# Kernel tuning notes

Hardware: AMD Instinct MI355X
Metric: run time of the kernel (lower is better)

The kernel has to match this reference:

```python
import jax, jax.numpy as jnp
import numpy as np
import math

H = 256; W = 256
NUM_CURVES = 256
NUM_SAMPLES = 32
NUM_BEZIERS = 2
BDEG = 5            # Bernstein degree used by the module (bezier_degree+1)
CTRL_STRIDE = 5     # bezier_degree+1; segments share endpoints, wrap (closed curve)
N_CTRL = NUM_BEZIERS * CTRL_STRIDE   # 10 control points per closed curve
PIX_CHUNK = 512
CHOLESKY_BOUND = jnp.array([0.5, 0.0, 0.5], jnp.float32)


def _bernstein():
    # t in linspace(0.007, 0.993, S) exactly as _update_bernstein_cache
    t = jnp.linspace(0.007, 0.993, NUM_SAMPLES)
    i = jnp.arange(BDEG + 1, dtype=jnp.float32)
    comb = jnp.array([math.comb(BDEG, k) for k in range(BDEG + 1)], jnp.float32)
    return comb * (t[:, None] ** i) * ((1.0 - t[:, None]) ** (BDEG - i))  # [S, BDEG+1]


def _render(control_points, features_dc, cholesky, opacity, depth, background):
    Bmat = _bernstein()
    # closed curve: segment k uses control points (k*5 + j) mod 10, j=0..5
    seg_idx = (jnp.arange(NUM_BEZIERS)[:, None] * CTRL_STRIDE
               + jnp.arange(BDEG + 1)[None, :]) % N_CTRL          # [K, 6]
    seg_ctrl = control_points[:, seg_idx]                          # [N, K, 6, 2]
    pts = jnp.einsum('sj,nkjd->nksd', Bmat, seg_ctrl)              # [N, K, S, 2]
    pts = pts.reshape(NUM_CURVES, -1, 2)                           # [N, Gper, 2]
    gper = pts.shape[1]

    # normalized [-1,1] -> pixel coords
    means = (jnp.tanh(pts) * 0.5 + 0.5) * jnp.array([W, H], jnp.float32)
    means = means.reshape(-1, 2)                                   # [G, 2]

    # 2x2 covariance from lower-triangular Cholesky (per curve)
    c = cholesky + CHOLESKY_BOUND[None, :]                         # l11, l21, l22
    s00 = c[:, 0] ** 2
    s01 = c[:, 0] * c[:, 1]
    s11 = c[:, 1] ** 2 + c[:, 2] ** 2
    det = s00 * s11 - s01 ** 2
    conic = jnp.stack([s11 / det, -s01 / det, s00 / det], -1)      # [N, 3]

    rep = lambda a: jnp.repeat(a, gper, axis=0)
    conic_g = rep(conic)                                           # [G, 3]
    color_g = rep(jax.nn.sigmoid(features_dc))                     # [G, 3]
    alpha_g = rep(jax.nn.sigmoid(opacity))[:, 0]                   # [G]
    depth_g = rep(depth)[:, 0]                                     # [G]

    order = jnp.argsort(depth_g)                                   # front-to-back
    means_s = means[order]
    conic_s = conic_g[order]
    color_s = color_g[order]
    alpha_s = alpha_g[order]

    ys, xs = jnp.meshgrid(jnp.arange(H, dtype=jnp.float32) + 0.5,
                          jnp.arange(W, dtype=jnp.float32) + 0.5, indexing='ij')
    pix = jnp.stack([xs.ravel(), ys.ravel()], -1).reshape(-1, PIX_CHUNK, 2)

    @jax.checkpoint
    def render_chunk(p):                                           # [C,2] -> [C,3]
        dx = p[:, None, 0] - means_s[None, :, 0]
        dy = p[:, None, 1] - means_s[None, :, 1]
        power = (-0.5 * (conic_s[None, :, 0] * dx * dx
                         + conic_s[None, :, 2] * dy * dy)
                 - conic_s[None, :, 1] * dx * dy)
        a = jnp.clip(alpha_s[None, :] * jnp.exp(power), 0.0, 0.999)
        logT = jnp.cumsum(jnp.log1p(-a), axis=1)
        t_excl = jnp.exp(logT - jnp.log1p(-a))   # transmittance before each splat
        rgb = (a * t_excl) @ color_s             # [C, 3]
        return rgb + jnp.exp(logT[:, -1:]) * background[None, :]

    img = jax.lax.map(render_chunk, pix)                           # [P/C, C, 3]
    return jnp.clip(img.reshape(H, W, 3), 0.0, 1.0)


def setup_inputs() -> dict:
    key = jax.random.key(0)
    k1, k2, k3, k4 = jax.random.split(key, 4)
    return {
        "control_points": jax.random.normal(k1, (NUM_CURVES, N_CTRL, 2), jnp.float32),
        "features_dc": jax.random.uniform(k2, (NUM_CURVES, 3), jnp.float32),
        "cholesky": jax.random.uniform(k3, (NUM_CURVES, 3), jnp.float32),
        "opacity": jnp.ones((NUM_CURVES, 1), jnp.float32),
        "depth": jax.random.uniform(k4, (NUM_CURVES, 1), jnp.float32),
        "background": jnp.ones((3,), jnp.float32),
    }


def reference(control_points, features_dc, cholesky, opacity, depth, background):
    return _render(control_points, features_dc, cholesky, opacity, depth, background)
```

## Files before the change

kernel.cpp:

```cpp
#include <hip/hip_runtime.h>
#include <hip/hip_fp16.h>
#include <math.h>

#define NCURVES   256
#define GPER      64
#define NUM_G     (NCURVES*GPER)
#define IMG_W     256
#define IMG_H     256
#define TILE      16
#define TILES_X   (IMG_W/TILE)
#define TILES_Y   (IMG_H/TILE)
#define NTILES    (TILES_X*TILES_Y)
#define REC_F     8

#define A_MIN     3.0e-6f
#define P_CUT     (-12.6f)

#define SEGS      8
#define GSEG      (NUM_G/SEGS)
#define GWAVE     (GSEG/4)

__global__ __launch_bounds__(GPER)
void prep(const float* __restrict__ ctrl,
          const float* __restrict__ features,
          const float* __restrict__ cholesky,
          const float* __restrict__ opacity,
          const float* __restrict__ depth,
          float*       __restrict__ recs,
          unsigned*    __restrict__ bbox)
{
    int c   = blockIdx.x;
    int tid = threadIdx.x;

    float dc = depth[c];
    int r = 0;
    #pragma unroll
    for (int jj = 0; jj < 4; ++jj) {
        int j = tid + jj*64;
        float dj = depth[j];
        r += (dj < dc) || (dj == dc && j < c);
    }
    #pragma unroll
    for (int off = 32; off > 0; off >>= 1) r += __shfl_down(r, off, 64);
    r = __shfl(r, 0, 64);

    float c0 = cholesky[3*c+0] + 0.5f;
    float c1 = cholesky[3*c+1];
    float c2 = cholesky[3*c+2] + 0.5f;
    float s00 = c0*c0;
    float s01 = c0*c1;
    float s11 = c1*c1 + c2*c2;
    float inv = 1.0f / (s00*s11 - s01*s01);
    float A  =  s11*inv;
    float Bc = -s01*inv;
    float Cc =  s00*inv;

    float cr = 1.0f/(1.0f + __expf(-features[3*c+0]));
    float cg = 1.0f/(1.0f + __expf(-features[3*c+1]));
    float cb = 1.0f/(1.0f + __expf(-features[3*c+2]));
    float al = 1.0f/(1.0f + __expf(-opacity[c]));

    float cut = fmaxf(2.0f*(__logf(al) - __logf(A_MIN)), 0.0f);
    float rx = sqrtf(cut * s00);
    float ry = sqrtf(cut * s11);

    int k = tid >> 5;
    int s = tid & 31;
    float t = 0.007f + (float)s * (0.986f/31.0f);
    float u = 1.0f - t;
    float t2=t*t, t3=t2*t, t4=t3*t, t5=t4*t;
    float u2=u*u, u3=u2*u, u4=u3*u, u5=u4*u;
    float w[6] = { u5, 5.0f*t*u4, 10.0f*t2*u3, 10.0f*t3*u2, 5.0f*t4*u, t5 };

    const float* cp = ctrl + c*20;
    float px = 0.0f, py = 0.0f;
    #pragma unroll
    for (int j = 0; j < 6; ++j) {
        int idx = (k*5 + j) % 10;
        px += w[j]*cp[2*idx+0];
        py += w[j]*cp[2*idx+1];
    }
    float mx = (tanhf(px)*0.5f + 0.5f) * (float)IMG_W;
    float my = (tanhf(py)*0.5f + 0.5f) * (float)IMG_H;

    int gi = r*GPER + tid;

    unsigned rg  = (unsigned)__half_as_ushort(__float2half_rn(cr))
                 | ((unsigned)__half_as_ushort(__float2half_rn(cg)) << 16);
    unsigned cbp = (unsigned)__half_as_ushort(__float2half_rn(cb));

    float4* o4 = (float4*)(recs + (size_t)gi*REC_F);
    o4[0] = make_float4(mx, my, A, Bc);
    o4[1] = make_float4(Cc, al, __uint_as_float(rg), __uint_as_float(cbp));

    int tx0 = min(max((int)floorf((mx - rx) * (1.0f/TILE)), 0), TILES_X-1);
    int tx1 = min(max((int)floorf((mx + rx) * (1.0f/TILE)), 0), TILES_X-1);
    int ty0 = min(max((int)floorf((my - ry) * (1.0f/TILE)), 0), TILES_Y-1);
    int ty1 = min(max((int)floorf((my + ry) * (1.0f/TILE)), 0), TILES_Y-1);
    bbox[gi] = (unsigned)tx0 | ((unsigned)ty0<<8) | ((unsigned)tx1<<16) | ((unsigned)ty1<<24);
}

__global__ __launch_bounds__(256)
void render8(const float*    __restrict__ recs,
             const unsigned* __restrict__ bbox,
             float4*         __restrict__ partial)
{
    __shared__ unsigned short flat[GSEG];
    __shared__ unsigned       wn[4];

    int tid   = threadIdx.x;
    int seg   = blockIdx.x & (SEGS-1);
    int tile  = blockIdx.x >> 3;
    int tilex = tile & (TILES_X-1);
    int tiley = tile >> 4;

    int lane = tid & 63;
    int wid  = tid >> 6;
    unsigned long long lmask = (1ull << lane) - 1ull;

    int sbase = seg * GSEG;
    int gwave = wid * GWAVE;

    bool pr[8];
    int cnt = 0;
    {
        unsigned bb[8];
        #pragma unroll
        for (int u = 0; u < 8; ++u)
            bb[u] = bbox[sbase + gwave + u*64 + lane];
        #pragma unroll
        for (int u = 0; u < 8; ++u) {
            unsigned b = bb[u];
            pr[u] = (tilex >= (int)( b        & 0xff)) &
                    (tilex <= (int)((b >> 16) & 0xff)) &
                    (tiley >= (int)((b >>  8) & 0xff)) &
                    (tiley <= (int)((b >> 24) & 0xff));
            cnt += (int)__popcll(__ballot(pr[u] ? 1 : 0));
        }
    }
    if (lane == 0) wn[wid] = (unsigned)cnt;
    __syncthreads();

    unsigned p1 = wn[0], p2 = p1 + wn[1], p3 = p2 + wn[2];
    int total = (int)(p3 + wn[3]);

    if (total) {
        unsigned base = (wid == 0) ? 0u : (wid == 1) ? p1 : (wid == 2) ? p2 : p3;
        int off = 0;
        #pragma unroll
        for (int u = 0; u < 8; ++u) {
            unsigned long long m = __ballot(pr[u] ? 1 : 0);
            if (pr[u])
                flat[base + off + (int)__popcll(m & lmask)] =
                    (unsigned short)(gwave + u*64 + lane);
            off += (int)__popcll(m);
        }
    }
    __syncthreads();

    int ix = tid & (TILE-1);
    int iy = tid >> 4;
    float pxf = (float)(tilex*TILE + ix) + 0.5f;
    float pyf = (float)(tiley*TILE + iy) + 0.5f;

    float T = 1.0f, accr = 0.0f, accg = 0.0f, accb = 0.0f;

    #pragma unroll 2
    for (int j = 0; j < total; ++j) {
        int gl = (int)flat[j];
        const float4* rp = (const float4*)(recs + (size_t)(sbase + gl)*REC_F);
        float4 r0 = rp[0];
        float4 r1 = rp[1];
        float dx = pxf - r0.x;
        float dy = pyf - r0.y;
        float p  = -0.5f*(r0.z*dx*dx + r1.x*dy*dy) - r0.w*dx*dy;
        if (p > P_CUT) {
            float a = fminf(r1.y * __expf(p), 0.999f);
            float wgt = a * T;
            unsigned rg = __float_as_uint(r1.z);
            accr += wgt * __half2float(__ushort_as_half((unsigned short)(rg & 0xffff)));
            accg += wgt * __half2float(__ushort_as_half((unsigned short)(rg >> 16)));
            accb += wgt * __half2float(__ushort_as_half((unsigned short)__float_as_uint(r1.w)));
            T *= (1.0f - a);
        }
    }

    int X = tilex*TILE + ix;
    int Y = tiley*TILE + iy;
    partial[(size_t)seg*(IMG_W*IMG_H) + (size_t)Y*IMG_W + X] =
        make_float4(accr, accg, accb, T);
}

__global__ __launch_bounds__(256)
void combine(const float4* __restrict__ partial,
             const float*  __restrict__ background,
             float*        __restrict__ out)
{
    int p = blockIdx.x * 256 + threadIdx.x;

    float accr = 0.0f, accg = 0.0f, accb = 0.0f, T = 1.0f;
    #pragma unroll
    for (int s = 0; s < SEGS; ++s) {
        float4 q = partial[(size_t)s*(IMG_W*IMG_H) + p];
        accr += T * q.x;
        accg += T * q.y;
        accb += T * q.z;
        T    *= q.w;
    }
    float r = fminf(fmaxf(accr + T*background[0], 0.0f), 1.0f);
    float g = fminf(fmaxf(accg + T*background[1], 0.0f), 1.0f);
    float b = fminf(fmaxf(accb + T*background[2], 0.0f), 1.0f);

    size_t oi = (size_t)p*3;
    out[oi+0] = r;
    out[oi+1] = g;
    out[oi+2] = b;
}

extern "C" void kernel_launch(void* const* d_in, const int* in_sizes, int n_in,
                              void* d_out, int out_size, void* d_ws, size_t ws_size,
                              hipStream_t stream)
{
    const float* ctrl       = (const float*)d_in[0];
    const float* features   = (const float*)d_in[1];
    const float* cholesky   = (const float*)d_in[2];
    const float* opacity    = (const float*)d_in[3];
    const float* depth      = (const float*)d_in[4];
    const float* background = (const float*)d_in[5];
    float* out = (float*)d_out;

    char* w = (char*)d_ws;
    float*    recs    = (float*)   (w);
    unsigned* bboxp   = (unsigned*)(w + 524288);
    float4*   partial = (float4*)  (w + 524288 + 65536);

    prep<<<NCURVES, GPER, 0, stream>>>(ctrl, features, cholesky, opacity, depth,
                                       recs, bboxp);
    render8<<<NTILES*SEGS, 256, 0, stream>>>(recs, bboxp, partial);
    combine<<<(IMG_W*IMG_H)/256, 256, 0, stream>>>(partial, background, out);
}
```

Before: 84.32 us.

## Software-pipeline record loads in render loop and exit early on saturation

The per-tile splat loop now processes records in groups of four, loading the next group into registers while the current group is composited, so global-load latency overlaps with math. The loop stops once every lane in the wave has transmittance below a small epsilon. The render kernel also gets a minimum-occupancy launch bound. The early exit drops contributions below the epsilon and may shift outputs slightly, and the prefetch buffers increase register pressure.

```diff
diff --git a/kernel.cpp b/kernel.cpp
--- a/kernel.cpp
+++ b/kernel.cpp
@@ -15,10 +15,12 @@
 
 #define A_MIN     3.0e-6f
 #define P_CUT     (-12.6f)
+#define T_EPS     1.0e-5f
 
 #define SEGS      8
 #define GSEG      (NUM_G/SEGS)
 #define GWAVE     (GSEG/4)
+#define PF        4
 
 __global__ __launch_bounds__(GPER)
 void prep(const float* __restrict__ ctrl,
@@ -100,7 +102,7 @@
     bbox[gi] = (unsigned)tx0 | ((unsigned)ty0<<8) | ((unsigned)tx1<<16) | ((unsigned)ty1<<24);
 }
 
-__global__ __launch_bounds__(256)
+__global__ __launch_bounds__(256, 4)
 void render8(const float*    __restrict__ recs,
              const unsigned* __restrict__ bbox,
              float4*         __restrict__ partial)
@@ -165,24 +167,51 @@
 
     float T = 1.0f, accr = 0.0f, accg = 0.0f, accb = 0.0f;
 
-    #pragma unroll 2
-    for (int j = 0; j < total; ++j) {
-        int gl = (int)flat[j];
-        const float4* rp = (const float4*)(recs + (size_t)(sbase + gl)*REC_F);
-        float4 r0 = rp[0];
-        float4 r1 = rp[1];
-        float dx = pxf - r0.x;
-        float dy = pyf - r0.y;
-        float p  = -0.5f*(r0.z*dx*dx + r1.x*dy*dy) - r0.w*dx*dy;
-        if (p > P_CUT) {
-            float a = fminf(r1.y * __expf(p), 0.999f);
-            float wgt = a * T;
-            unsigned rg = __float_as_uint(r1.z);
-            accr += wgt * __half2float(__ushort_as_half((unsigned short)(rg & 0xffff)));
-            accg += wgt * __half2float(__ushort_as_half((unsigned short)(rg >> 16)));
-            accb += wgt * __half2float(__ushort_as_half((unsigned short)__float_as_uint(r1.w)));
-            T *= (1.0f - a);
-        }
+    float4 c0[PF], c1[PF], n0[PF], n1[PF];
+
+    #pragma unroll
+    for (int u = 0; u < PF; ++u) {
+        if (u < total) {
+            const float4* rp = (const float4*)
+                (recs + (size_t)(sbase + (int)flat[u])*REC_F);
+            c0[u] = rp[0]; c1[u] = rp[1];
+        }
+    }
+
+    #pragma unroll 1
+    for (int base = 0; base < total; base += PF) {
+        int nb = base + PF;
+        #pragma unroll
+        for (int u = 0; u < PF; ++u) {
+            if (nb + u < total) {
+                const float4* rp = (const float4*)
+                    (recs + (size_t)(sbase + (int)flat[nb + u])*REC_F);
+                n0[u] = rp[0]; n1[u] = rp[1];
+            }
+        }
+        #pragma unroll
+        for (int u = 0; u < PF; ++u) {
+            if (base + u < total) {
+                float4 r0 = c0[u];
+                float4 r1 = c1[u];
+                float dx = pxf - r0.x;
+                float dy = pyf - r0.y;
+                float p  = -0.5f*(r0.z*dx*dx + r1.x*dy*dy) - r0.w*dx*dy;
+                if (p > P_CUT) {
+                    float a = fminf(r1.y * __expf(p), 0.999f);
+                    float wgt = a * T;
+                    unsigned rg = __float_as_uint(r1.z);
+                    accr += wgt * __half2float(__ushort_as_half((unsigned short)(rg & 0xffff)));
+                    accg += wgt * __half2float(__ushort_as_half((unsigned short)(rg >> 16)));
+                    accb += wgt * __half2float(__ushort_as_half((unsigned short)__float_as_uint(r1.w)));
+                    T *= (1.0f - a);
+                }
+            }
+        }
+        #pragma unroll
+        for (int u = 0; u < PF; ++u) { c0[u] = n0[u]; c1[u] = n1[u]; }
+
+        if (!__any(T > T_EPS)) break;
     }
 
     int X = tilex*TILE + ix;
```

Measured after the change: 87.60 us. +3.9%, slower.

## Render 8x8 tiles with per-wave depth quarters and in-block combine

Applied to the files above, without the earlier changes.

Shrinks tiles to 8x8 so each of the four waves in a block covers the same 64 pixels, with each wave taking a quarter of the depth-sorted splats. The four partial results are composited in shared memory, which removes the separate combine kernel and the global partial buffer. Each wave also exits early once every lane's transmittance falls below a small epsilon. In exchange each block scans a quarter of all bboxes per wave, and early termination adds a tiny approximation.

```diff
diff --git a/kernel.cpp b/kernel.cpp
--- a/kernel.cpp
+++ b/kernel.cpp
@@ -7,7 +7,7 @@
 #define NUM_G     (NCURVES*GPER)
 #define IMG_W     256
 #define IMG_H     256
-#define TILE      16
+#define TILE      8
 #define TILES_X   (IMG_W/TILE)
 #define TILES_Y   (IMG_H/TILE)
 #define NTILES    (TILES_X*TILES_Y)
@@ -15,10 +15,10 @@
 
 #define A_MIN     3.0e-6f
 #define P_CUT     (-12.6f)
-
-#define SEGS      8
-#define GSEG      (NUM_G/SEGS)
-#define GWAVE     (GSEG/4)
+#define T_EPS     1.0e-5f
+
+#define WQ        4
+#define GQ        (NUM_G/WQ)
 
 __global__ __launch_bounds__(GPER)
 void prep(const float* __restrict__ ctrl,
@@ -101,74 +101,55 @@
 }
 
 __global__ __launch_bounds__(256)
-void render8(const float*    __restrict__ recs,
-             const unsigned* __restrict__ bbox,
-             float4*         __restrict__ partial)
+void render8x8(const float*    __restrict__ recs,
+               const unsigned* __restrict__ bbox,
+               const float*    __restrict__ background,
+               float*          __restrict__ out)
 {
-    __shared__ unsigned short flat[GSEG];
-    __shared__ unsigned       wn[4];
+    __shared__ unsigned short lst[WQ][GQ];
+    __shared__ float4         pc[WQ][64];
 
     int tid   = threadIdx.x;
-    int seg   = blockIdx.x & (SEGS-1);
-    int tile  = blockIdx.x >> 3;
+    int lane  = tid & 63;
+    int w     = tid >> 6;
+    int tile  = blockIdx.x;
     int tilex = tile & (TILES_X-1);
-    int tiley = tile >> 4;
-
-    int lane = tid & 63;
-    int wid  = tid >> 6;
+    int tiley = tile >> 5;
     unsigned long long lmask = (1ull << lane) - 1ull;
 
-    int sbase = seg * GSEG;
-    int gwave = wid * GWAVE;
-
-    bool pr[8];
+    int gb = w * GQ;
+
     int cnt = 0;
-    {
+    #pragma unroll 1
+    for (int b = 0; b < 8; ++b) {
         unsigned bb[8];
         #pragma unroll
         for (int u = 0; u < 8; ++u)
-            bb[u] = bbox[sbase + gwave + u*64 + lane];
+            bb[u] = bbox[gb + (b*8 + u)*64 + lane];
         #pragma unroll
         for (int u = 0; u < 8; ++u) {
-            unsigned b = bb[u];
-            pr[u] = (tilex >= (int)( b        & 0xff)) &
-                    (tilex <= (int)((b >> 16) & 0xff)) &
-                    (tiley >= (int)((b >>  8) & 0xff)) &
-                    (tiley <= (int)((b >> 24) & 0xff));
-            cnt += (int)__popcll(__ballot(pr[u] ? 1 : 0));
+            unsigned v = bb[u];
+            bool pred = (tilex >= (int)( v        & 0xff)) &
+                        (tilex <= (int)((v >> 16) & 0xff)) &
+                        (tiley >= (int)((v >>  8) & 0xff)) &
+                        (tiley <= (int)((v >> 24) & 0xff));
+            unsigned long long m = __ballot(pred ? 1 : 0);
+            if (pred)
+                lst[w][cnt + (int)__popcll(m & lmask)] =
+                    (unsigned short)((b*8 + u)*64 + lane);
+            cnt += (int)__popcll(m);
         }
     }
-    if (lane == 0) wn[wid] = (unsigned)cnt;
-    __syncthreads();
-
-    unsigned p1 = wn[0], p2 = p1 + wn[1], p3 = p2 + wn[2];
-    int total = (int)(p3 + wn[3]);
-
-    if (total) {
-        unsigned base = (wid == 0) ? 0u : (wid == 1) ? p1 : (wid == 2) ? p2 : p3;
-        int off = 0;
-        #pragma unroll
-        for (int u = 0; u < 8; ++u) {
-            unsigned long long m = __ballot(pr[u] ? 1 : 0);
-            if (pr[u])
-                flat[base + off + (int)__popcll(m & lmask)] =
-                    (unsigned short)(gwave + u*64 + lane);
-            off += (int)__popcll(m);
-        }
-    }
-    __syncthreads();
-
-    int ix = tid & (TILE-1);
-    int iy = tid >> 4;
-    float pxf = (float)(tilex*TILE + ix) + 0.5f;
-    float pyf = (float)(tiley*TILE + iy) + 0.5f;
+
+    float pxf = (float)(tilex*TILE + (lane & 7)) + 0.5f;
+    float pyf = (float)(tiley*TILE + (lane >> 3)) + 0.5f;
 
     float T = 1.0f, accr = 0.0f, accg = 0.0f, accb = 0.0f;
 
     #pragma unroll 2
-    for (int j = 0; j < total; ++j) {
-        int gl = (int)flat[j];
-        const float4* rp = (const float4*)(recs + (size_t)(sbase + gl)*REC_F);
+    for (int j = 0; j < cnt; ++j) {
+        int g = gb + (int)lst[w][j];
+        const float4* rp = (const float4*)(recs + (size_t)g*REC_F);
         float4 r0 = rp[0];
         float4 r1 = rp[1];
         float dx = pxf - r0.x;
@@ -183,38 +164,33 @@
             accb += wgt * __half2float(__ushort_as_half((unsigned short)__float_as_uint(r1.w)));
             T *= (1.0f - a);
         }
-    }
-
-    int X = tilex*TILE + ix;
-    int Y = tiley*TILE + iy;
-    partial[(size_t)seg*(IMG_W*IMG_H) + (size_t)Y*IMG_W + X] =
-        make_float4(accr, accg, accb, T);
-}
-
-__global__ __launch_bounds__(256)
-void combine(const float4* __restrict__ partial,
-             const float*  __restrict__ background,
-             float*        __restrict__ out)
-{
-    int p = blockIdx.x * 256 + threadIdx.x;
-
-    float accr = 0.0f, accg = 0.0f, accb = 0.0f, T = 1.0f;
-    #pragma unroll
-    for (int s = 0; s < SEGS; ++s) {
-        float4 q = partial[(size_t)s*(IMG_W*IMG_H) + p];
-        accr += T * q.x;
-        accg += T * q.y;
-        accb += T * q.z;
-        T    *= q.w;
-    }
-    float r = fminf(fmaxf(accr + T*background[0], 0.0f), 1.0f);
-    float g = fminf(fmaxf(accg + T*background[1], 0.0f), 1.0f);
-    float b = fminf(fmaxf(accb + T*background[2], 0.0f), 1.0f);
-
-    size_t oi = (size_t)p*3;
-    out[oi+0] = r;
-    out[oi+1] = g;
-    out[oi+2] = b;
+        if (!__any(T > T_EPS)) break;
+    }
+
+    pc[w][lane] = make_float4(accr, accg, accb, T);
+    __syncthreads();
+
+    if (w == 0) {
+        float4 a0 = pc[0][lane];
+        float4 a1 = pc[1][lane];
+        float4 a2 = pc[2][lane];
+        float4 a3 = pc[3][lane];
+        float r = a0.x + a0.w*(a1.x + a1.w*(a2.x + a2.w*a3.x));
+        float g = a0.y + a0.w*(a1.y + a1.w*(a2.y + a2.w*a3.y));
+        float b = a0.z + a0.w*(a1.z + a1.w*(a2.z + a2.w*a3.z));
+        float Tt = a0.w * a1.w * a2.w * a3.w;
+
+        r = fminf(fmaxf(r + Tt*background[0], 0.0f), 1.0f);
+        g = fminf(fmaxf(g + Tt*background[1], 0.0f), 1.0f);
+        b = fminf(fmaxf(b + Tt*background[2], 0.0f), 1.0f);
+
+        int X = tilex*TILE + (lane & 7);
+        int Y = tiley*TILE + (lane >> 3);
+        size_t oi = ((size_t)Y*IMG_W + X)*3;
+        out[oi+0] = r;
+        out[oi+1] = g;
+        out[oi+2] = b;
+    }
 }
 
 extern "C" void kernel_launch(void* const* d_in, const int* in_sizes, int n_in,
@@ -230,12 +206,10 @@
     float* out = (float*)d_out;
 
     char* w = (char*)d_ws;
-    float*    recs    = (float*)   (w);
-    unsigned* bboxp   = (unsigned*)(w + 524288);
-    float4*   partial = (float4*)  (w + 524288 + 65536);
+    float*    recs  = (float*)   (w);
+    unsigned* bboxp = (unsigned*)(w + 524288);
 
     prep<<<NCURVES, GPER, 0, stream>>>(ctrl, features, cholesky, opacity, depth,
                                        recs, bboxp);
-    render8<<<NTILES*SEGS, 256, 0, stream>>>(recs, bboxp, partial);
-    combine<<<(IMG_W*IMG_H)/256, 256, 0, stream>>>(partial, background, out);
+    render8x8<<<NTILES, 256, 0, stream>>>(recs, bboxp, background, out);
 }
```

New measurement: 95.28 us. 13.0% more time.

## Stage splat records in shared memory and terminate early on saturated transmittance

Applied to the files above, without the earlier changes.

The render loop now loads blocks of up to 512 candidate splat records cooperatively into LDS, and all pixels read them from there. Before, every thread fetched each record from global memory on its own. It also adds block-level and wave-level early exit once transmittance drops below 1e-5, which skips splats that would contribute almost nothing. The cost is 16KB of extra LDS per block, which may lower occupancy, plus extra barriers. The early exit changes results slightly, since it ignores contributions below the epsilon.

```diff
diff --git a/kernel.cpp b/kernel.cpp
--- a/kernel.cpp
+++ b/kernel.cpp
@@ -15,10 +15,12 @@
 
 #define A_MIN     3.0e-6f
 #define P_CUT     (-12.6f)
+#define T_EPS     1.0e-5f
 
 #define SEGS      8
 #define GSEG      (NUM_G/SEGS)
 #define GWAVE     (GSEG/4)
+#define STAGE     512
 
 __global__ __launch_bounds__(GPER)
 void prep(const float* __restrict__ ctrl,
@@ -106,6 +108,7 @@
              float4*         __restrict__ partial)
 {
     __shared__ unsigned short flat[GSEG];
+    __shared__ float4         sd[STAGE][2];
     __shared__ unsigned       wn[4];
 
     int tid   = threadIdx.x;
@@ -165,24 +168,45 @@
 
     float T = 1.0f, accr = 0.0f, accg = 0.0f, accb = 0.0f;
 
-    #pragma unroll 2
-    for (int j = 0; j < total; ++j) {
-        int gl = (int)flat[j];
-        const float4* rp = (const float4*)(recs + (size_t)(sbase + gl)*REC_F);
-        float4 r0 = rp[0];
-        float4 r1 = rp[1];
-        float dx = pxf - r0.x;
-        float dy = pyf - r0.y;
-        float p  = -0.5f*(r0.z*dx*dx + r1.x*dy*dy) - r0.w*dx*dy;
-        if (p > P_CUT) {
-            float a = fminf(r1.y * __expf(p), 0.999f);
-            float wgt = a * T;
-            unsigned rg = __float_as_uint(r1.z);
-            accr += wgt * __half2float(__ushort_as_half((unsigned short)(rg & 0xffff)));
-            accg += wgt * __half2float(__ushort_as_half((unsigned short)(rg >> 16)));
-            accb += wgt * __half2float(__ushort_as_half((unsigned short)__float_as_uint(r1.w)));
-            T *= (1.0f - a);
-        }
+    #pragma unroll 1
+    for (int base = 0; base < total; base += STAGE) {
+        int nalive = __syncthreads_count(T > T_EPS);
+        if (nalive == 0) break;
+
+        int nstage = total - base;
+        if (nstage > STAGE) nstage = STAGE;
+
+        for (int e = tid; e < nstage; e += 256) {
+            int g = sbase + (int)flat[base + e];
+            const float4* rp = (const float4*)(recs + (size_t)g*REC_F);
+            sd[e][0] = rp[0];
+            sd[e][1] = rp[1];
+        }
+        __syncthreads();
+
+        #pragma unroll 1
+        for (int jb = 0; jb < nstage; jb += 32) {
+            if (!__any(T > T_EPS)) break;
+            int je = jb + 32 < nstage ? jb + 32 : nstage;
+            #pragma unroll 4
+            for (int j = jb; j < je; ++j) {
+                float4 r0 = sd[j][0];
+                float4 r1 = sd[j][1];
+                float dx = pxf - r0.x;
+                float dy = pyf - r0.y;
+                float p  = -0.5f*(r0.z*dx*dx + r1.x*dy*dy) - r0.w*dx*dy;
+                if (p > P_CUT) {
+                    float a = fminf(r1.y * __expf(p), 0.999f);
+                    float wgt = a * T;
+                    unsigned rg = __float_as_uint(r1.z);
+                    accr += wgt * __half2float(__ushort_as_half((unsigned short)(rg & 0xffff)));
+                    accg += wgt * __half2float(__ushort_as_half((unsigned short)(rg >> 16)));
+                    accb += wgt * __half2float(__ushort_as_half((unsigned short)__float_as_uint(r1.w)));
+                    T *= (1.0f - a);
+                }
+            }
+        }
+        __syncthreads();
     }
 
     int X = tilex*TILE + ix;
```

Result: no change. 83.14 us (-1.4%).
